# Optimization experiments

Hardware: AMD Instinct MI355X
Metric: run time of the kernel (lower is better)

The kernel has to match this reference:

```python
import jax, jax.numpy as jnp
import numpy as np

SMALL = -1000.0


def setup_inputs() -> dict:
    key = jax.random.key(0)
    k1, k2, k3, k4 = jax.random.split(key, 4)
    B, T, L = 1024, 512, 62          # batch, max_seq_len, emission label count
    K = L + 2                         # total labels incl. start (L) and end (L+1)
    pred = jax.random.normal(k1, (B, T, L), dtype=jnp.float32)
    ref = jax.random.randint(k2, (B, T), 0, L)
    seq_len = jnp.clip(jax.random.randint(k3, (B,), 0, T + 1), 1, T)
    transitions = jax.random.normal(k4, (K, K), dtype=jnp.float32)
    transitions = transitions.at[K - 2, :].set(-10000.0)
    transitions = transitions.at[K - 1, :].set(-10000.0)
    return {"pred": pred, "ref": ref, "seq_len": seq_len, "transitions": transitions}


def _crf_loss(pred, ref, seq_len, transitions):
    B, T, L = pred.shape
    K = L + 2
    start_id, end_id = L, L + 1
    dt = pred.dtype

    # observations: (B, T+2, K) = [b_s row, padded emissions, right padding row]
    obs = jnp.concatenate([pred, jnp.full((B, T, 2), SMALL, dtype=dt)], axis=2)
    b_s = jnp.concatenate([jnp.full((L,), SMALL, dt), jnp.array([0.0, SMALL], dt)])
    r_pad = jnp.concatenate([jnp.zeros((L,), dt), jnp.full((2,), SMALL, dt)])
    observations = jnp.concatenate(
        [jnp.broadcast_to(b_s, (B, 1, K)), obs, jnp.broadcast_to(r_pad, (B, 1, K))],
        axis=1)
    # end-of-sequence bonus added at position seq_len+1 for each example
    e_s = jnp.concatenate([jnp.full((L,), SMALL, dt), jnp.array([0.0, 1000.0], dt)])
    observations = observations.at[jnp.arange(B), seq_len + 1].add(e_s)

    # sequential forward (alpha) recurrence: logsumexp over previous label
    def step(prev, obs_t):
        # prev: (B, K), obs_t: (B, K); scores: (B, K_prev, K_next)
        scores = prev[:, :, None] + obs_t[:, None, :] + transitions
        new = jax.nn.logsumexp(scores, axis=1)
        return new, new

    init = observations[:, 0]                              # (B, K)
    xs = jnp.swapaxes(observations[:, 1:, :], 0, 1)        # (T+1, B, K)
    _, paths_scores = jax.lax.scan(step, init, xs)         # (T+1, B, K)

    final = paths_scores[seq_len, jnp.arange(B)]           # (B, K) alpha at step seq_len
    all_paths_scores = jax.nn.logsumexp(final, axis=1).sum()

    # gold path emission score
    emit_mask = (jnp.arange(T)[None, :] < seq_len[:, None]).astype(dt)   # (B, T)
    gold_emit = jnp.take_along_axis(pred, ref[:, :, None], axis=2)[..., 0]
    real_score = jnp.sum(gold_emit * emit_mask)

    # gold path transition score: [start, tags..., end]
    padded = jnp.concatenate(
        [jnp.full((B, 1), start_id, ref.dtype), ref, jnp.zeros((B, 1), ref.dtype)],
        axis=1)                                            # (B, T+2)
    padded = padded.at[jnp.arange(B), seq_len + 1].set(end_id)
    trans_mask = (jnp.arange(T + 1)[None, :] < (seq_len + 1)[:, None]).astype(dt)
    gold_trans = transitions[padded[:, :-1], padded[:, 1:]]  # (B, T+1)
    real_score = real_score + jnp.sum(gold_trans * trans_mask)

    return all_paths_scores - real_score


def reference(pred, ref, seq_len, transitions):
    return _crf_loss(pred, ref, seq_len, transitions)
```

## Files before the change

### kernel.cpp

```cpp
#include <hip/hip_runtime.h>


#define SMALLF   (-1000.0f)
#define LOG2E_F  1.4426950408889634f
#define LN2_F    0.6931471805599453f

#if defined(__has_builtin)
#if __has_builtin(__builtin_amdgcn_exp2f)
#define EXP2F(x) __builtin_amdgcn_exp2f(x)
#else
#define EXP2F(x) exp2f(x)
#endif
#if __has_builtin(__builtin_amdgcn_logf)
#define LOG2F(x) __builtin_amdgcn_logf(x)
#else
#define LOG2F(x) log2f(x)
#endif
#else
#define EXP2F(x) exp2f(x)
#define LOG2F(x) log2f(x)
#endif

typedef _Float16 h2 __attribute__((ext_vector_type(2)));

#if defined(__has_builtin) && __has_builtin(__builtin_amdgcn_fdot2)
#define FDOT2(a, b, c) __builtin_amdgcn_fdot2((a), (b), (c), false)
#else
#define FDOT2(a, b, c) fmaf((float)(a).x, (float)(b).x, \
                            fmaf((float)(a).y, (float)(b).y, (c)))
#endif

template <int CTRL>
__device__ __forceinline__ unsigned dppmov(unsigned v) {
    return (unsigned)__builtin_amdgcn_update_dpp((int)v, (int)v, CTRL, 0xF, 0xF, false);
}
#define DPP_QP_X1 0xB1
#define DPP_QP_X2 0x4E
#define DPP_ROR4  0x124
#define DPP_ROR8  0x128
#define DPP_ROR12 0x12C

__device__ __forceinline__ unsigned x4sel(unsigned v, bool b2) {
    const unsigned a = dppmov<DPP_ROR4>(v);
    const unsigned b = dppmov<DPP_ROR12>(v);
    return b2 ? a : b;
}

__device__ __forceinline__ unsigned x16(unsigned v, bool sel) {
    unsigned a = v, b = v;
    asm("v_permlane16_swap_b32 %0, %1" : "+v"(a), "+v"(b));
    return sel ? a : b;
}
__device__ __forceinline__ unsigned x32(unsigned v, bool sel) {
    unsigned a = v, b = v;
    asm("v_permlane32_swap_b32 %0, %1" : "+v"(a), "+v"(b));
    return sel ? a : b;
}

__device__ __forceinline__ float bcast_first(float v) {
    return __uint_as_float(__builtin_amdgcn_readfirstlane(__float_as_uint(v)));
}

__device__ __forceinline__ float step_scale(float ss, int& Ci) {
    const float s0 = bcast_first(ss);
    const int ex = (int)((__float_as_uint(s0) >> 23) & 0xFF) - 127;
    Ci += ex + 6;
    return __uint_as_float((unsigned)(127 - ex - 6) << 23);
}

__device__ __forceinline__ float step_ss(float hf,
                                         const h2* __restrict__ EhA,
                                         const h2* __restrict__ EhB,
                                         const h2* __restrict__ EhC,
                                         const h2* __restrict__ EhD,
                                         bool b2, bool s16, bool s32) {
    const unsigned n1 = dppmov<DPP_QP_X1>(__float_as_uint(hf));
    unsigned r[8];
    r[0] = __builtin_bit_cast(unsigned,
              __builtin_amdgcn_cvt_pkrtz(hf, __uint_as_float(n1)));
    r[1] = dppmov<DPP_QP_X2>(r[0]);
    r[2] = x4sel(r[0], b2);
    r[3] = x4sel(r[1], b2);
    r[4] = dppmov<DPP_ROR8>(r[0]);
    r[5] = dppmov<DPP_ROR8>(r[1]);
    r[6] = dppmov<DPP_ROR8>(r[2]);
    r[7] = dppmov<DPP_ROR8>(r[3]);
    float pA = 0.f, pB = 0.f, pC = 0.f, pD = 0.f;
#pragma unroll
    for (int k = 0; k < 8; ++k) {
        const h2 v = __builtin_bit_cast(h2, r[k]);
        pA = FDOT2(v, EhA[k], pA);
        pB = FDOT2(v, EhB[k], pB);
        pC = FDOT2(v, EhC[k], pC);
        pD = FDOT2(v, EhD[k], pD);
    }
    const float A  = pA + __uint_as_float(x16(__float_as_uint(pB), s16));
    const float A2 = pC + __uint_as_float(x16(__float_as_uint(pD), s16));
    return A + __uint_as_float(x32(__float_as_uint(A2), s32));
}

__global__ __launch_bounds__(64, 1) void crf_fused_kernel(
    const float* __restrict__ pred,
    const int*   __restrict__ ref,
    const int*   __restrict__ seq_len,
    const float* __restrict__ trans,
    float*       __restrict__ out,
    int T, int L)
{
    const int b    = blockIdx.x;
    const unsigned lane = threadIdx.x;
    const int slen = seq_len[b];
    const int nmid = slen - 1;
    const float* prow = pred + (size_t)b * T * L;
    const int*   rrow = ref  + (size_t)b * T;
    const bool mine = (lane < 62);

    int cidx[8], pidx[8];
#pragma unroll
    for (int k = 0; k < 8; ++k) {
        const int t = (int)lane + (k << 6);
        cidx[k] = (t < slen) ? rrow[t] : 0;
        pidx[k] = (t >= 1 && t < slen) ? rrow[t - 1] : 0;
    }
    float gacc = 0.f;
#pragma unroll
    for (int k = 0; k < 8; ++k) {
        const int t = (int)lane + (k << 6);
        if (t < slen) {
            gacc += prow[(size_t)t * L + cidx[k]];
            if (t >= 1) gacc += trans[(pidx[k] << 6) + cidx[k]];
        }
    }
    if (lane == 0)
        gacc += trans[(62 << 6) + rrow[0]] + trans[(rrow[slen - 1] << 6) + 63];

    const bool b2 = (lane & 4u) != 0;
    bool flip16 = false, flip32 = false;
    {
        const unsigned p = x16(lane, ((lane >> 4) & 1u) != 0);
        if (__builtin_amdgcn_readfirstlane((int)p) == 0) flip16 = true;
        const unsigned q = x32(lane, ((lane >> 5) & 1u) != 0);
        if (__builtin_amdgcn_readfirstlane((int)q) == 0) flip32 = true;
    }
    const bool s16 = ((((lane >> 4) & 1u) != 0) != flip16);
    const bool s32 = ((((lane >> 5) & 1u) != 0) != flip32);
    const unsigned m16 = x16(lane, s16);
    const unsigned m32 = x32(lane, s32);
    const unsigned cD  = x16(m32, s16);

    unsigned gp[8];
    gp[0] = lane | (dppmov<DPP_QP_X1>(lane) << 16);
    gp[1] = dppmov<DPP_QP_X2>(gp[0]);
    gp[2] = x4sel(gp[0], b2);
    gp[3] = x4sel(gp[1], b2);
    gp[4] = dppmov<DPP_ROR8>(gp[0]);
    gp[5] = dppmov<DPP_ROR8>(gp[1]);
    gp[6] = dppmov<DPP_ROR8>(gp[2]);
    gp[7] = dppmov<DPP_ROR8>(gp[3]);

    h2 EhA[8], EhB[8], EhC[8], EhD[8];
    float sA = 0.f, sB = 0.f, sC = 0.f, sD = 0.f;
#pragma unroll
    for (int k = 0; k < 8; ++k) {
        const unsigned rlo = gp[k] & 0xFFFFu;
        const unsigned rhi = gp[k] >> 16;
        const float a0 = EXP2F(trans[rlo * 64u + lane] * LOG2E_F);
        const float a1 = EXP2F(trans[rhi * 64u + lane] * LOG2E_F);
        EhA[k].x = (_Float16)a0; EhA[k].y = (_Float16)a1; sA += a0 + a1;
        const float b0 = EXP2F(trans[rlo * 64u + m16] * LOG2E_F);
        const float b1 = EXP2F(trans[rhi * 64u + m16] * LOG2E_F);
        EhB[k].x = (_Float16)b0; EhB[k].y = (_Float16)b1; sB += b0 + b1;
        const float c0 = EXP2F(trans[rlo * 64u + m32] * LOG2E_F);
        const float c1 = EXP2F(trans[rhi * 64u + m32] * LOG2E_F);
        EhC[k].x = (_Float16)c0; EhC[k].y = (_Float16)c1; sC += c0 + c1;
        const float d0 = EXP2F(trans[rlo * 64u + cD] * LOG2E_F);
        const float d1 = EXP2F(trans[rhi * 64u + cD] * LOG2E_F);
        EhD[k].x = (_Float16)d0; EhD[k].y = (_Float16)d1; sD += d0 + d1;
    }
    const float psA  = sA + __uint_as_float(x16(__float_as_uint(sB), s16));
    const float psA2 = sC + __uint_as_float(x16(__float_as_uint(sD), s16));
    const float psum = psA + __uint_as_float(x32(__float_as_uint(psA2), s32));

    float cur[8];
#pragma unroll
    for (int u = 0; u < 8; ++u) {
        const int row = (u + 1 < T) ? (u + 1) : (T - 1);
        cur[u] = mine ? prow[(size_t)row * L + lane] : 0.f;
    }

    int Ci = 0;
    const float c_base = SMALLF * LOG2E_F;
    float hf;
    {
        const float q0 = psum * EXP2F((mine ? prow[lane] : 0.f) * LOG2E_F);
        const float sc = step_scale(q0, Ci);
        hf = q0 * sc;
    }

    const int nfull = nmid >> 3;
    const int rem   = nmid & 7;
    for (int c = 0; c < nfull; ++c) {
        float W[8], nxt[8];
#pragma unroll
        for (int u = 0; u < 8; ++u)
            W[u] = EXP2F(cur[u] * LOG2E_F);
        const int base = 8 * (c + 1) + 1;
#pragma unroll
        for (int u = 0; u < 8; ++u) {
            const int row = (base + u < T) ? (base + u) : (T - 1);
            nxt[u] = mine ? prow[(size_t)row * L + lane] : 0.f;
        }
#pragma unroll
        for (int u = 0; u < 8; ++u) {
            const float ss = step_ss(hf, EhA, EhB, EhC, EhD, b2, s16, s32);
            const float sc = step_scale(ss, Ci);
            hf = ss * (W[u] * sc);
        }
#pragma unroll
        for (int u = 0; u < 8; ++u) cur[u] = nxt[u];
    }

    float Wr[7];
#pragma unroll
    for (int u = 0; u < 7; ++u)
        Wr[u] = EXP2F(cur[u] * LOG2E_F);
#pragma unroll
    for (int u = 0; u < 7; ++u) {
        if (u < rem) {
            const float ss = step_ss(hf, EhA, EhB, EhC, EhD, b2, s16, s32);
            const float sc = step_scale(ss, Ci);
            hf = ss * (Wr[u] * sc);
        }
    }

    {
        const float ssf = step_ss(hf, EhA, EhB, EhC, EhD, b2, s16, s32);
        const float pvf = (slen < T) ? cur[rem] : 0.f;
        float ob;
        if (lane < 62)       ob = pvf + SMALLF;
        else if (lane == 62) ob = SMALLF;
        else                 ob = 0.f;
        const float alpha = c_base + (float)Ci + LOG2F(ssf) + ob * LOG2E_F;

        float mx = alpha;
#pragma unroll
        for (int k = 32; k >= 1; k >>= 1)
            mx = fmaxf(mx, __shfl_xor(mx, k, 64));
        float pe = EXP2F(alpha - mx);
#pragma unroll
        for (int k = 32; k >= 1; k >>= 1)
            pe += __shfl_xor(pe, k, 64);
#pragma unroll
        for (int k = 32; k >= 1; k >>= 1)
            gacc += __shfl_xor(gacc, k, 64);

        if (lane == 0) {
            const float logZ2 = mx + LOG2F(pe);
            atomicAdd(out, LN2_F * logZ2 - gacc);
        }
    }
}

extern "C" void kernel_launch(void* const* d_in, const int* in_sizes, int n_in,
                              void* d_out, int out_size, void* d_ws, size_t ws_size,
                              hipStream_t stream) {
    const float* pred  = (const float*)d_in[0];
    const int*   ref   = (const int*)  d_in[1];
    const int*   slen  = (const int*)  d_in[2];
    const float* trans = (const float*)d_in[3];

    const int B = in_sizes[2];
    const int T = in_sizes[1] / B;
    const int L = in_sizes[0] / in_sizes[1];

    hipMemsetAsync(d_out, 0, sizeof(float), stream);
    crf_fused_kernel<<<B, 64, 0, stream>>>(pred, ref, slen, trans,
                                           (float*)d_out, T, L);
}
```

Measured before the change: 265.4 us.

## Split CRF partition recurrence into concurrent forward and backward halves meeting midway

Replaces the single serial forward scan with a forward recurrence and a backward (beta) recurrence that each run half the sequence in interleaved steps, then combines them with a dot product to get the partition function. This roughly halves the length of the latency-bound dependent chain, since two independent chains can overlap within one wavefront. It also restructures the matvec to hold all 32 transition-weight pairs per lane, using permlane swaps of the state instead of partial-sum swaps, which raises register use. The backward path needs the transposed exp-transition table and changes edge handling for the end label and short sequences.

```diff
diff --git a/kernel.cpp b/kernel.cpp
--- a/kernel.cpp
+++ b/kernel.cpp
@@ -46,16 +46,8 @@
     return b2 ? a : b;
 }
 
-__device__ __forceinline__ unsigned x16(unsigned v, bool sel) {
-    unsigned a = v, b = v;
-    asm("v_permlane16_swap_b32 %0, %1" : "+v"(a), "+v"(b));
-    return sel ? a : b;
-}
-__device__ __forceinline__ unsigned x32(unsigned v, bool sel) {
-    unsigned a = v, b = v;
-    asm("v_permlane32_swap_b32 %0, %1" : "+v"(a), "+v"(b));
-    return sel ? a : b;
-}
+#define SWAP16(a, b) asm("v_permlane16_swap_b32 %0, %1" : "+v"(a), "+v"(b))
+#define SWAP32(a, b) asm("v_permlane32_swap_b32 %0, %1" : "+v"(a), "+v"(b))
 
 __device__ __forceinline__ float bcast_first(float v) {
     return __uint_as_float(__builtin_amdgcn_readfirstlane(__float_as_uint(v)));
@@ -69,13 +61,10 @@
 }
 
 __device__ __forceinline__ float step_ss(float hf,
-                                         const h2* __restrict__ EhA,
-                                         const h2* __restrict__ EhB,
-                                         const h2* __restrict__ EhC,
-                                         const h2* __restrict__ EhD,
-                                         bool b2, bool s16, bool s32) {
+                                         const h2* __restrict__ Eh,
+                                         bool b2) {
+    unsigned r[32];
     const unsigned n1 = dppmov<DPP_QP_X1>(__float_as_uint(hf));
-    unsigned r[8];
     r[0] = __builtin_bit_cast(unsigned,
               __builtin_amdgcn_cvt_pkrtz(hf, __uint_as_float(n1)));
     r[1] = dppmov<DPP_QP_X2>(r[0]);
@@ -85,18 +74,17 @@
     r[5] = dppmov<DPP_ROR8>(r[1]);
     r[6] = dppmov<DPP_ROR8>(r[2]);
     r[7] = dppmov<DPP_ROR8>(r[3]);
-    float pA = 0.f, pB = 0.f, pC = 0.f, pD = 0.f;
-#pragma unroll
-    for (int k = 0; k < 8; ++k) {
-        const h2 v = __builtin_bit_cast(h2, r[k]);
-        pA = FDOT2(v, EhA[k], pA);
-        pB = FDOT2(v, EhB[k], pB);
-        pC = FDOT2(v, EhC[k], pC);
-        pD = FDOT2(v, EhD[k], pD);
-    }
-    const float A  = pA + __uint_as_float(x16(__float_as_uint(pB), s16));
-    const float A2 = pC + __uint_as_float(x16(__float_as_uint(pD), s16));
-    return A + __uint_as_float(x32(__float_as_uint(A2), s32));
+#pragma unroll
+    for (int k = 0; k < 8; ++k) { r[8 + k] = r[k]; SWAP16(r[k], r[8 + k]); }
+#pragma unroll
+    for (int k = 0; k < 16; ++k) { r[16 + k] = r[k]; SWAP32(r[k], r[16 + k]); }
+    float a[8];
+#pragma unroll
+    for (int j = 0; j < 8; ++j) a[j] = 0.f;
+#pragma unroll
+    for (int k = 0; k < 32; ++k)
+        a[k & 7] = FDOT2(__builtin_bit_cast(h2, r[k]), Eh[k], a[k & 7]);
+    return ((a[0] + a[1]) + (a[2] + a[3])) + ((a[4] + a[5]) + (a[6] + a[7]));
 }
 
 __global__ __launch_bounds__(64, 1) void crf_fused_kernel(
@@ -114,6 +102,7 @@
     const float* prow = pred + (size_t)b * T * L;
     const int*   rrow = ref  + (size_t)b * T;
     const bool mine = (lane < 62);
+    const bool b2 = (lane & 4u) != 0;
 
     int cidx[8], pidx[8];
 #pragma unroll
@@ -134,21 +123,7 @@
     if (lane == 0)
         gacc += trans[(62 << 6) + rrow[0]] + trans[(rrow[slen - 1] << 6) + 63];
 
-    const bool b2 = (lane & 4u) != 0;
-    bool flip16 = false, flip32 = false;
-    {
-        const unsigned p = x16(lane, ((lane >> 4) & 1u) != 0);
-        if (__builtin_amdgcn_readfirstlane((int)p) == 0) flip16 = true;
-        const unsigned q = x32(lane, ((lane >> 5) & 1u) != 0);
-        if (__builtin_amdgcn_readfirstlane((int)q) == 0) flip32 = true;
-    }
-    const bool s16 = ((((lane >> 4) & 1u) != 0) != flip16);
-    const bool s32 = ((((lane >> 5) & 1u) != 0) != flip32);
-    const unsigned m16 = x16(lane, s16);
-    const unsigned m32 = x32(lane, s32);
-    const unsigned cD  = x16(m32, s16);
-
-    unsigned gp[8];
+    unsigned gp[32];
     gp[0] = lane | (dppmov<DPP_QP_X1>(lane) << 16);
     gp[1] = dppmov<DPP_QP_X2>(gp[0]);
     gp[2] = x4sel(gp[0], b2);
@@ -157,105 +132,102 @@
     gp[5] = dppmov<DPP_ROR8>(gp[1]);
     gp[6] = dppmov<DPP_ROR8>(gp[2]);
     gp[7] = dppmov<DPP_ROR8>(gp[3]);
-
-    h2 EhA[8], EhB[8], EhC[8], EhD[8];
-    float sA = 0.f, sB = 0.f, sC = 0.f, sD = 0.f;
-#pragma unroll
-    for (int k = 0; k < 8; ++k) {
+#pragma unroll
+    for (int k = 0; k < 8; ++k) { gp[8 + k] = gp[k]; SWAP16(gp[k], gp[8 + k]); }
+#pragma unroll
+    for (int k = 0; k < 16; ++k) { gp[16 + k] = gp[k]; SWAP32(gp[k], gp[16 + k]); }
+
+    h2 Eh_f[32], Eh_b[32];
+    float psum = 0.f;
+#pragma unroll
+    for (int k = 0; k < 32; ++k) {
         const unsigned rlo = gp[k] & 0xFFFFu;
         const unsigned rhi = gp[k] >> 16;
-        const float a0 = EXP2F(trans[rlo * 64u + lane] * LOG2E_F);
-        const float a1 = EXP2F(trans[rhi * 64u + lane] * LOG2E_F);
-        EhA[k].x = (_Float16)a0; EhA[k].y = (_Float16)a1; sA += a0 + a1;
-        const float b0 = EXP2F(trans[rlo * 64u + m16] * LOG2E_F);
-        const float b1 = EXP2F(trans[rhi * 64u + m16] * LOG2E_F);
-        EhB[k].x = (_Float16)b0; EhB[k].y = (_Float16)b1; sB += b0 + b1;
-        const float c0 = EXP2F(trans[rlo * 64u + m32] * LOG2E_F);
-        const float c1 = EXP2F(trans[rhi * 64u + m32] * LOG2E_F);
-        EhC[k].x = (_Float16)c0; EhC[k].y = (_Float16)c1; sC += c0 + c1;
-        const float d0 = EXP2F(trans[rlo * 64u + cD] * LOG2E_F);
-        const float d1 = EXP2F(trans[rhi * 64u + cD] * LOG2E_F);
-        EhD[k].x = (_Float16)d0; EhD[k].y = (_Float16)d1; sD += d0 + d1;
-    }
-    const float psA  = sA + __uint_as_float(x16(__float_as_uint(sB), s16));
-    const float psA2 = sC + __uint_as_float(x16(__float_as_uint(sD), s16));
-    const float psum = psA + __uint_as_float(x32(__float_as_uint(psA2), s32));
-
-    float cur[8];
-#pragma unroll
-    for (int u = 0; u < 8; ++u) {
-        const int row = (u + 1 < T) ? (u + 1) : (T - 1);
-        cur[u] = mine ? prow[(size_t)row * L + lane] : 0.f;
-    }
-
-    int Ci = 0;
+        const float f0 = EXP2F(trans[rlo * 64u + lane] * LOG2E_F);
+        const float f1 = EXP2F(trans[rhi * 64u + lane] * LOG2E_F);
+        Eh_f[k].x = (_Float16)f0; Eh_f[k].y = (_Float16)f1;
+        psum += f0 + f1;
+        const float g0 = EXP2F(trans[lane * 64u + rlo] * LOG2E_F);
+        const float g1 = EXP2F(trans[lane * 64u + rhi] * LOG2E_F);
+        Eh_b[k].x = (_Float16)g0; Eh_b[k].y = (_Float16)g1;
+    }
+
+    const int fwd_mid = nmid >> 1;
+    const int bwd_mid = nmid - fwd_mid;
+    const int common  = fwd_mid;
+
+    float cur_f[4], cur_b[4];
+#pragma unroll
+    for (int u = 0; u < 4; ++u) {
+        const int rf = (u + 1 < T) ? (u + 1) : (T - 1);
+        cur_f[u] = mine ? prow[(size_t)rf * L + lane] : 0.f;
+        int rb = slen - 2 - u; rb = (rb > 0) ? rb : 0;
+        cur_b[u] = mine ? prow[(size_t)rb * L + lane] : 0.f;
+    }
+    const float pv_b0 = mine ? prow[(size_t)(slen - 1) * L + lane] : 0.f;
+
+    int Ci_f = 0, Ci_b = 0;
     const float c_base = SMALLF * LOG2E_F;
-    float hf;
+    float hf, hb;
     {
         const float q0 = psum * EXP2F((mine ? prow[lane] : 0.f) * LOG2E_F);
-        const float sc = step_scale(q0, Ci);
+        const float sc = step_scale(q0, Ci_f);
         hf = q0 * sc;
     }
-
-    const int nfull = nmid >> 3;
-    const int rem   = nmid & 7;
-    for (int c = 0; c < nfull; ++c) {
-        float W[8], nxt[8];
-#pragma unroll
-        for (int u = 0; u < 8; ++u)
-            W[u] = EXP2F(cur[u] * LOG2E_F);
-        const int base = 8 * (c + 1) + 1;
-#pragma unroll
-        for (int u = 0; u < 8; ++u) {
-            const int row = (base + u < T) ? (base + u) : (T - 1);
-            nxt[u] = mine ? prow[(size_t)row * L + lane] : 0.f;
-        }
-#pragma unroll
-        for (int u = 0; u < 8; ++u) {
-            const float ss = step_ss(hf, EhA, EhB, EhC, EhD, b2, s16, s32);
-            const float sc = step_scale(ss, Ci);
-            hf = ss * (W[u] * sc);
-        }
-#pragma unroll
-        for (int u = 0; u < 8; ++u) cur[u] = nxt[u];
-    }
-
-    float Wr[7];
-#pragma unroll
-    for (int u = 0; u < 7; ++u)
-        Wr[u] = EXP2F(cur[u] * LOG2E_F);
-#pragma unroll
-    for (int u = 0; u < 7; ++u) {
-        if (u < rem) {
-            const float ss = step_ss(hf, EhA, EhB, EhC, EhD, b2, s16, s32);
-            const float sc = step_scale(ss, Ci);
-            hf = ss * (Wr[u] * sc);
-        }
-    }
-
     {
-        const float ssf = step_ss(hf, EhA, EhB, EhC, EhD, b2, s16, s32);
-        const float pvf = (slen < T) ? cur[rem] : 0.f;
-        float ob;
-        if (lane < 62)       ob = pvf + SMALLF;
-        else if (lane == 62) ob = SMALLF;
-        else                 ob = 0.f;
-        const float alpha = c_base + (float)Ci + LOG2F(ssf) + ob * LOG2E_F;
-
-        float mx = alpha;
+        const float Elast = EXP2F(trans[lane * 64u + 63u] * LOG2E_F);
+        const float Wb0 = (bwd_mid > 0) ? (mine ? EXP2F(pv_b0 * LOG2E_F) : 0.f)
+                                        : 1.0f;
+        hb = Elast * Wb0;
+    }
+
+    for (int m0 = 0; m0 < common; m0 += 4) {
+        float Wf[4], Wbn[4], nf[4], nb[4];
+#pragma unroll
+        for (int u = 0; u < 4; ++u) {
+            Wf[u]  = EXP2F(cur_f[u] * LOG2E_F);
+            Wbn[u] = mine ? EXP2F(cur_b[u] * LOG2E_F) : 0.f;
+        }
+#pragma unroll
+        for (int u = 0; u < 4; ++u) {
+            int rf = m0 + 5 + u; rf = (rf < T) ? rf : (T - 1);
+            nf[u] = mine ? prow[(size_t)rf * L + lane] : 0.f;
+            int rb = slen - 6 - m0 - u; rb = (rb > 0) ? rb : 0;
+            nb[u] = mine ? prow[(size_t)rb * L + lane] : 0.f;
+        }
+#pragma unroll
+        for (int u = 0; u < 4; ++u) {
+            if (m0 + u < common) {
+                const float ssf = step_ss(hf, Eh_f, b2);
+                const float ssb = step_ss(hb, Eh_b, b2);
+                const float scf = step_scale(ssf, Ci_f);
+                const float scb = step_scale(ssb, Ci_b);
+                hf = ssf * (Wf[u] * scf);
+                const float wN = (m0 + u + 1 < bwd_mid) ? Wbn[u] : 1.0f;
+                hb = ssb * (wN * scb);
+            }
+        }
+#pragma unroll
+        for (int u = 0; u < 4; ++u) { cur_f[u] = nf[u]; cur_b[u] = nb[u]; }
+    }
+
+    if (bwd_mid > common) {
+        const float ssb = step_ss(hb, Eh_b, b2);
+        const float scb = step_scale(ssb, Ci_b);
+        hb = ssb * scb;
+    }
+
+    {
+        float p = hf * hb;
 #pragma unroll
         for (int k = 32; k >= 1; k >>= 1)
-            mx = fmaxf(mx, __shfl_xor(mx, k, 64));
-        float pe = EXP2F(alpha - mx);
-#pragma unroll
-        for (int k = 32; k >= 1; k >>= 1)
-            pe += __shfl_xor(pe, k, 64);
+            p += __shfl_xor(p, k, 64);
 #pragma unroll
         for (int k = 32; k >= 1; k >>= 1)
             gacc += __shfl_xor(gacc, k, 64);
 
         if (lane == 0) {
-            const float logZ2 = mx + LOG2F(pe);
+            const float logZ2 = c_base + (float)(Ci_f + Ci_b) + LOG2F(p);
             atomicAdd(out, LN2_F * logZ2 - gacc);
         }
     }
```

Result: slower. 329.3 us (+24.1%).
